# Kernel optimization log

Hardware: AMD Instinct MI355X
Metric: run time of the kernel (lower is better)

Reference implementation:

```python
import jax, jax.numpy as jnp
import numpy as np

N_NODES = 100000


def _gcn_conv(x, W, b, src, dst, n_nodes):
    # PyG GCNConv: linear transform, add self-loops, symmetric deg normalization,
    # scatter-add aggregation at target nodes, then bias.
    h = x @ W  # [N, out]
    loops = jnp.arange(n_nodes, dtype=src.dtype)
    src2 = jnp.concatenate([src, loops])
    dst2 = jnp.concatenate([dst, loops])
    ones = jnp.ones(src2.shape[0], dtype=h.dtype)
    deg = jax.ops.segment_sum(ones, dst2, num_segments=n_nodes)  # in-degree incl. self-loop
    dinv = jnp.where(deg > 0, jax.lax.rsqrt(deg), 0.0)
    norm = dinv[src2] * dinv[dst2]  # [E+N]
    msg = h[src2] * norm[:, None]  # gather + weight, [E+N, out]
    out = jax.ops.segment_sum(msg, dst2, num_segments=n_nodes)
    return out + b


def setup_inputs() -> dict:
    key = jax.random.key(0)
    k1, k2, k3, k4 = jax.random.split(key, 4)
    n, e, f, h, c = N_NODES, 3200000, 512, 16, 32
    x = jax.random.normal(k1, (n, f), dtype=jnp.float32)
    edge_index = jax.random.randint(k2, (2, e), 0, n, dtype=jnp.int64)
    W1 = jax.random.normal(k3, (f, h), dtype=jnp.float32) * (1.0 / np.sqrt(f))
    b1 = jnp.zeros((h,), dtype=jnp.float32)
    W2 = jax.random.normal(k4, (h, c), dtype=jnp.float32) * (1.0 / np.sqrt(h))
    b2 = jnp.zeros((c,), dtype=jnp.float32)
    return {"x": x, "edge_index": edge_index, "W1": W1, "b1": b1, "W2": W2, "b2": b2}


def reference(x, edge_index, W1, b1, W2, b2):
    src, dst = edge_index[0], edge_index[1]
    n = x.shape[0]
    h = _gcn_conv(x, W1, b1, src, dst, n)
    h = jax.nn.relu(h)
    h = _gcn_conv(h, W2, b2, src, dst, n)
    return jax.nn.log_softmax(h, axis=1)
```

## Files before the change

kernel.cpp:

```cpp
#include <hip/hip_runtime.h>
#include <hip/hip_bf16.h>


#define BK 128
#define BKSH 7
#define MAXNB 1024
#define CHUNK 12800

typedef __attribute__((ext_vector_type(8))) short bf16x8;
typedef __attribute__((ext_vector_type(4))) float f32x4;

__device__ __forceinline__ short f2b(float f) {
    unsigned u = __float_as_uint(f);
    return (short)((u + 0x7FFF + ((u >> 16) & 1)) >> 16);
}
__device__ __forceinline__ float b2f(unsigned short s) {
    return __uint_as_float(((unsigned)s) << 16);
}

__device__ __forceinline__ void load_lds16(const float* g, void* l) {
    __builtin_amdgcn_global_load_lds((const __attribute__((address_space(1))) void*)g,
                                     (__attribute__((address_space(3))) void*)l, 16, 0, 0);
}

__global__ __launch_bounds__(256) void k_zero_i(int* __restrict__ p, int n) {
    int i = blockIdx.x * 256 + threadIdx.x;
    if (i < n) p[i] = 0;
}

__global__ __launch_bounds__(256) void k_hist(const int* __restrict__ dst,
                                              int* __restrict__ gcnt, int E, int NB) {
    __shared__ int h[MAXNB];
    for (int t = threadIdx.x; t < NB; t += 256) h[t] = 0;
    __syncthreads();
    int e0 = blockIdx.x * CHUNK, e1 = min(E, e0 + CHUNK);
    for (int e = e0 + threadIdx.x; e < e1; e += 256)
        atomicAdd(&h[dst[e] >> BKSH], 1);
    __syncthreads();
    for (int t = threadIdx.x; t < NB; t += 256)
        if (h[t]) atomicAdd(&gcnt[t], h[t]);
}

__global__ __launch_bounds__(1024) void k_scan_nb(const int* __restrict__ gcnt,
                                                  int* __restrict__ goffs,
                                                  int* __restrict__ gcur, int NB, int E) {
    __shared__ int sm[1024];
    int tid = threadIdx.x;
    int c = (tid < NB) ? gcnt[tid] : 0;
    sm[tid] = c;
    __syncthreads();
    for (int o = 1; o < 1024; o <<= 1) {
        int t = (tid >= o) ? sm[tid - o] : 0;
        __syncthreads();
        sm[tid] += t;
        __syncthreads();
    }
    if (tid < NB) { int v = sm[tid] - c; goffs[tid] = v; gcur[tid] = v; }
    if (tid == 0) goffs[NB] = E;
}

__global__ __launch_bounds__(256) void k_fill2(const int* __restrict__ src,
                                               const int* __restrict__ dst,
                                               int* __restrict__ gcur,
                                               int* __restrict__ gq, int E, int NB) {
    __shared__ int h[MAXNB];
    __shared__ int base[MAXNB];
    for (int t = threadIdx.x; t < NB; t += 256) h[t] = 0;
    __syncthreads();
    int e0 = blockIdx.x * CHUNK, e1 = min(E, e0 + CHUNK);
    for (int e = e0 + threadIdx.x; e < e1; e += 256)
        atomicAdd(&h[dst[e] >> BKSH], 1);
    __syncthreads();
    for (int t = threadIdx.x; t < NB; t += 256) {
        int c = h[t];
        base[t] = c ? atomicAdd(&gcur[t], c) : 0;
    }
    __syncthreads();
    for (int t = threadIdx.x; t < NB; t += 256) h[t] = 0;
    __syncthreads();
    for (int e = e0 + threadIdx.x; e < e1; e += 256) {
        int d = dst[e], b = d >> BKSH;
        int loc = atomicAdd(&h[b], 1);
        gq[base[b] + loc] = (src[e] << BKSH) | (d & (BK - 1));
    }
}

__global__ __launch_bounds__(256) void k_sortb(const int* __restrict__ gq,
                                               const int* __restrict__ goffs,
                                               int* __restrict__ gq2,
                                               int* __restrict__ offs,
                                               float* __restrict__ dinv,
                                               int n, int E) {
    __shared__ int cnt[BK];
    __shared__ int cur[BK];
    int b = blockIdx.x;
    if (threadIdx.x < BK) cnt[threadIdx.x] = 0;
    __syncthreads();
    int p0 = goffs[b], p1 = goffs[b + 1];
    for (int p = p0 + threadIdx.x; p < p1; p += 256)
        atomicAdd(&cnt[gq[p] & (BK - 1)], 1);
    __syncthreads();
    if (threadIdx.x < BK) cur[threadIdx.x] = cnt[threadIdx.x];
    __syncthreads();
    for (int o = 1; o < BK; o <<= 1) {
        int v = (threadIdx.x < BK && threadIdx.x >= o) ? cur[threadIdx.x - o] : 0;
        __syncthreads();
        if (threadIdx.x < BK) cur[threadIdx.x] += v;
        __syncthreads();
    }
    if (threadIdx.x < BK) {
        int excl = cur[threadIdx.x] - cnt[threadIdx.x];
        int node = (b << BKSH) + threadIdx.x;
        if (node < n) {
            offs[node] = p0 + excl;
            dinv[node] = rsqrtf((float)(cnt[threadIdx.x] + 1));
        }
        cur[threadIdx.x] = excl;
    }
    if (b == 0 && threadIdx.x == 0) offs[n] = E;
    __syncthreads();
    for (int p = p0 + threadIdx.x; p < p1; p += 256) {
        int e = gq[p];
        int loc = atomicAdd(&cur[e & (BK - 1)], 1);
        gq2[p0 + loc] = e;
    }
}

__global__ __launch_bounds__(256) void k_gemm_mfma(const float* __restrict__ x,
                                                   const float* __restrict__ W1,
                                                   const float* __restrict__ dinv,
                                                   unsigned short* __restrict__ gs1,
                                                   int n) {
    const int lane = threadIdx.x & 63;
    const int r = lane & 15;
    const int g4 = lane >> 4;
    const int wid = blockIdx.x * 4 + (threadIdx.x >> 6);
    const int nw = gridDim.x * 4;

    bf16x8 wf[16];
#pragma unroll
    for (int s = 0; s < 16; ++s) {
        int kb = s * 32 + g4 * 8;
#pragma unroll
        for (int j = 0; j < 8; ++j)
            wf[s][j] = f2b(W1[(size_t)(kb + j) * 16 + r]);
    }

    const int ntiles = (n + 15) >> 4;
    for (int tile = wid; tile < ntiles; tile += nw) {
        int m0 = tile << 4;
        int arow = m0 + r;
        if (arow >= n) arow = n - 1;
        const float* xp = x + (size_t)arow * 512 + g4 * 8;
        f32x4 acc = {0.f, 0.f, 0.f, 0.f};
#pragma unroll
        for (int s = 0; s < 16; ++s) {
            float4 f0 = *reinterpret_cast<const float4*>(xp + s * 32);
            float4 f1 = *reinterpret_cast<const float4*>(xp + s * 32 + 4);
            bf16x8 ah;
            ah[0] = f2b(f0.x); ah[1] = f2b(f0.y); ah[2] = f2b(f0.z); ah[3] = f2b(f0.w);
            ah[4] = f2b(f1.x); ah[5] = f2b(f1.y); ah[6] = f2b(f1.z); ah[7] = f2b(f1.w);
            acc = __builtin_amdgcn_mfma_f32_16x16x32_bf16(ah, wf[s], acc, 0, 0, 0);
        }
#pragma unroll
        for (int j = 0; j < 4; ++j) {
            int crow = m0 + g4 * 4 + j;
            if (crow < n) {
                float dvv = dinv[crow];
                gs1[(size_t)crow * 16 + r] = (unsigned short)f2b(acc[j] * dvv);
            }
        }
    }
}

__global__ __launch_bounds__(256) void k_agg_b(const unsigned short* __restrict__ featb,
                                               const int* __restrict__ gq2,
                                               const int* __restrict__ offs,
                                               const float* __restrict__ dinv,
                                               const float* __restrict__ bias,
                                               unsigned short* __restrict__ out_b,
                                               float* __restrict__ out_f,
                                               int n, int relu_flag) {
    int t = blockIdx.x * 256 + threadIdx.x;
    int i = t >> 4, k = t & 15;
    if (i >= n) return;
    float acc = b2f(featb[(size_t)i * 16 + k]);
    int p = offs[i], p1 = offs[i + 1];
    for (; p + 4 <= p1; p += 4) {
        int s0 = gq2[p] >> BKSH, s1 = gq2[p + 1] >> BKSH;
        int s2 = gq2[p + 2] >> BKSH, s3 = gq2[p + 3] >> BKSH;
        float v0 = b2f(featb[(size_t)s0 * 16 + k]);
        float v1 = b2f(featb[(size_t)s1 * 16 + k]);
        float v2 = b2f(featb[(size_t)s2 * 16 + k]);
        float v3 = b2f(featb[(size_t)s3 * 16 + k]);
        acc += v0 + v1 + v2 + v3;
    }
    for (; p < p1; ++p)
        acc += b2f(featb[(size_t)(gq2[p] >> BKSH) * 16 + k]);
    float dvi = dinv[i];
    float v = dvi * acc;
    if (relu_flag) {
        v = fmaxf(v + bias[k], 0.f) * dvi;
        out_b[(size_t)i * 16 + k] = (unsigned short)f2b(v);
    } else {
        out_f[(size_t)i * 16 + k] = v;
    }
}

__global__ __launch_bounds__(256) void k_out(const float* __restrict__ a,
                                             const float* __restrict__ W2,
                                             const float* __restrict__ b2,
                                             float* __restrict__ out, int n) {
    __shared__ float Ws[16 * 33];
    __shared__ float bs[32];
    for (int t = threadIdx.x; t < 512; t += 256) Ws[(t >> 5) * 33 + (t & 31)] = W2[t];
    if (threadIdx.x < 32) bs[threadIdx.x] = b2[threadIdx.x];
    __syncthreads();
    int t = blockIdx.x * 256 + threadIdx.x;
    int i = t >> 5, c = t & 31;
    if (i >= n) return;
    const float4* ar = reinterpret_cast<const float4*>(a + (size_t)i * 16);
    float acc = bs[c];
#pragma unroll
    for (int kk = 0; kk < 4; ++kk) {
        float4 v = ar[kk];
        acc += v.x * Ws[(4 * kk + 0) * 33 + c];
        acc += v.y * Ws[(4 * kk + 1) * 33 + c];
        acc += v.z * Ws[(4 * kk + 2) * 33 + c];
        acc += v.w * Ws[(4 * kk + 3) * 33 + c];
    }
    float m = acc;
#pragma unroll
    for (int o = 16; o > 0; o >>= 1) m = fmaxf(m, __shfl_xor(m, o, 32));
    float p = expf(acc - m);
#pragma unroll
    for (int o = 16; o > 0; o >>= 1) p += __shfl_xor(p, o, 32);
    out[t] = acc - m - logf(p);
}

__global__ __launch_bounds__(256) void k_count(const int* __restrict__ dst,
                                               int* __restrict__ cnt, int E) {
    int e = blockIdx.x * 256 + threadIdx.x;
    if (e < E) atomicAdd(&cnt[dst[e]], 1);
}

__global__ __launch_bounds__(256) void k_dinv(const int* __restrict__ cnt,
                                              float* __restrict__ dinv, int n) {
    int i = blockIdx.x * 256 + threadIdx.x;
    if (i < n) dinv[i] = rsqrtf((float)(cnt[i] + 1));
}

__global__ __launch_bounds__(256) void k_gemm1(const float* __restrict__ x,
                                               const float* __restrict__ W1,
                                               const float* __restrict__ dinv,
                                               float* __restrict__ h1,
                                               float* __restrict__ r1self, int n) {
    __shared__ float Ws[8192];
    __shared__ float4 Xs[4][512];
    for (int t = threadIdx.x; t < 8192; t += 256) {
        int sa = t ^ (((t >> 9) & 1) << 4);
        Ws[sa] = W1[t];
    }
    __syncthreads();
    const int wave = threadIdx.x >> 6;
    const int lane = threadIdx.x & 63;
    const int q = lane & 15, g = lane >> 4;
    const int sr = lane >> 3, su = lane & 7;
    const int first = blockIdx.x * 4 + wave;
    const int stride = gridDim.x * 4;
    const int ngroups = (n + 7) >> 3;
    if (first >= ngroups) return;
    const int mygroups = (ngroups - first + stride - 1) / stride;
    const int T = mygroups * 4;
    char* xbase = (char*)(&Xs[wave][0]);
    auto stage = [&](int i) {
        int k = i >> 2, c = i & 3;
        int r0 = (first + k * stride) << 3;
        int row = r0 + sr;
        if (row >= n) row = n - 1;
        const float* gp = x + (size_t)row * 512 + c * 128 + su * 4;
        char* lb = xbase + (i & 1) * 4096;
#pragma unroll
        for (int m = 0; m < 4; ++m) load_lds16(gp + m * 32, lb + m * 1024);
    };
    stage(0);
    if (T > 1) stage(1);
    int issued = (T > 1) ? 2 : 1;
    float acc[8];
    const float4* xw = &Xs[wave][0];
    const int flip = (g & 1) << 4;
    for (int i = 0; i < T; ++i) {
        if (i < T - 1) asm volatile("s_waitcnt vmcnt(4)" ::: "memory");
        else           asm volatile("s_waitcnt vmcnt(0)" ::: "memory");
        int c = i & 3;
        const float4* xb = xw + (i & 1) * 256;
        if (c == 0) {
#pragma unroll
            for (int r = 0; r < 8; ++r) acc[r] = 0.f;
        }
        const int aW = 2048 * c + 512 * g + q;
#pragma unroll
        for (int t = 0; t < 8; ++t) {
            int tg = (t + g) & 7;
            float4 xv[8];
#pragma unroll
            for (int r = 0; r < 8; ++r) xv[r] = xb[g * 64 + r * 8 + tg];
            int a0 = aW + 64 * tg;
            float w0 = Ws[(a0) ^ flip];
            float w1 = Ws[(a0 + 16) ^ flip];
            float w2 = Ws[(a0 + 32) ^ flip];
            float w3 = Ws[(a0 + 48) ^ flip];
#pragma unroll
            for (int r = 0; r < 8; ++r)
                acc[r] += xv[r].x * w0 + xv[r].y * w1 + xv[r].z * w2 + xv[r].w * w3;
        }
        if (issued < T) { stage(issued); ++issued; }
        if (c == 3) {
            int r0 = (first + (i >> 2) * stride) << 3;
#pragma unroll
            for (int r = 0; r < 8; ++r) {
                acc[r] += __shfl_xor(acc[r], 16);
                acc[r] += __shfl_xor(acc[r], 32);
            }
            float v0 = 0.f, v1 = 0.f;
#pragma unroll
            for (int r = 0; r < 4; ++r)
                if (g == r) { v0 = acc[r]; v1 = acc[r + 4]; }
            int row0 = r0 + g, row1 = r0 + 4 + g;
            if (row0 < n) {
                h1[(size_t)row0 * 16 + q] = v0;
                if (r1self) { float dv = dinv[row0]; r1self[(size_t)row0 * 16 + q] = v0 * dv * dv; }
            }
            if (row1 < n) {
                h1[(size_t)row1 * 16 + q] = v1;
                if (r1self) { float dv = dinv[row1]; r1self[(size_t)row1 * 16 + q] = v1 * dv * dv; }
            }
        }
    }
}

__global__ __launch_bounds__(256) void k_scatter16(const int* __restrict__ src,
                                                   const int* __restrict__ dst,
                                                   const float* __restrict__ feat,
                                                   const float* __restrict__ dinv,
                                                   float* __restrict__ outf, int total) {
    int t = blockIdx.x * 256 + threadIdx.x;
    if (t >= total) return;
    int e = t >> 4, k = t & 15;
    int s = src[e], d = dst[e];
    float w = dinv[s] * dinv[d];
    unsafeAtomicAdd(&outf[(size_t)d * 16 + k], feat[(size_t)s * 16 + k] * w);
}

__global__ __launch_bounds__(256) void k_relu16(float* __restrict__ r1,
                                                const float* __restrict__ b1, int total) {
    int t = blockIdx.x * 256 + threadIdx.x;
    if (t < total) r1[t] = fmaxf(r1[t] + b1[t & 15], 0.f);
}

__global__ __launch_bounds__(256) void k_self16(const float* __restrict__ feat,
                                                const float* __restrict__ dinv,
                                                float* __restrict__ outf, int total) {
    int t = blockIdx.x * 256 + threadIdx.x;
    if (t >= total) return;
    float dv = dinv[t >> 4];
    outf[t] = feat[t] * dv * dv;
}

extern "C" void kernel_launch(void* const* d_in, const int* in_sizes, int n_in,
                              void* d_out, int out_size, void* d_ws, size_t ws_size,
                              hipStream_t stream) {
    const float* x  = (const float*)d_in[0];
    const int* ei   = (const int*)d_in[1];
    const float* W1 = (const float*)d_in[2];
    const float* b1 = (const float*)d_in[3];
    const float* W2 = (const float*)d_in[4];
    const float* b2 = (const float*)d_in[5];
    float* out = (float*)d_out;

    const int n = in_sizes[0] / 512;
    const int E = in_sizes[1] / 2;
    const int* src = ei;
    const int* dst = ei + E;
    const int NB = (n + BK - 1) >> BKSH;
    const int gfill = (E + CHUNK - 1) / CHUNK;

    float* ws = (float*)d_ws;

    size_t u_dinv  = 0;
    size_t u_foffs = u_dinv + n;
    size_t u_goffs = u_foffs + n + 1;
    size_t u_gcnt  = u_goffs + NB + 1;
    size_t u_gcur  = u_gcnt + NB;
    size_t u_gq    = u_gcur + NB;
    size_t u_gq2   = u_gq + (size_t)E;
    size_t u_h1    = u_gq2 + (size_t)E;
    size_t u_r1    = u_h1 + 16 * (size_t)n;
    size_t need    = (u_r1 + 16 * (size_t)n) * 4;

    if (ws_size >= need && NB <= MAXNB) {
        float* dinv = ws + u_dinv;
        int* offs   = (int*)(ws + u_foffs);
        int* goffs  = (int*)(ws + u_goffs);
        int* gcnt   = (int*)(ws + u_gcnt);
        int* gcur   = (int*)(ws + u_gcur);
        int* gq     = (int*)(ws + u_gq);
        int* gq2    = (int*)(ws + u_gq2);
        unsigned short* gs1b = (unsigned short*)(ws + u_h1);
        unsigned short* r1sb = (unsigned short*)(ws + u_r1);
        float* a_f  = ws + u_h1;

        k_zero_i <<<(NB + 255) / 256, 256, 0, stream>>>(gcnt, NB);
        k_hist   <<<gfill, 256, 0, stream>>>(dst, gcnt, E, NB);
        k_scan_nb<<<1, 1024, 0, stream>>>(gcnt, goffs, gcur, NB, E);
        k_fill2  <<<gfill, 256, 0, stream>>>(src, dst, gcur, gq, E, NB);
        k_sortb  <<<NB, 256, 0, stream>>>(gq, goffs, gq2, offs, dinv, n, E);
        k_gemm_mfma<<<1024, 256, 0, stream>>>(x, W1, dinv, gs1b, n);
        k_agg_b  <<<(n * 16 + 255) / 256, 256, 0, stream>>>(gs1b, gq2, offs, dinv, b1,
                                                            r1sb, nullptr, n, 1);
        k_agg_b  <<<(n * 16 + 255) / 256, 256, 0, stream>>>(r1sb, gq2, offs, dinv, b1,
                                                            nullptr, a_f, n, 0);
        k_out    <<<(n * 32 + 255) / 256, 256, 0, stream>>>(a_f, W2, b2, out, n);
    } else {
        float* dinv = ws;
        float* h1   = ws + n;
        float* r1   = ws + n + 16 * (size_t)n;
        int* cnt    = (int*)h1;
        float* agg2r = h1;

        const int total1 = E * 16;
        k_zero_i   <<<(n + 255) / 256, 256, 0, stream>>>(cnt, n);
        k_count    <<<(E + 255) / 256, 256, 0, stream>>>(dst, cnt, E);
        k_dinv     <<<(n + 255) / 256, 256, 0, stream>>>(cnt, dinv, n);
        k_gemm1    <<<1024, 256, 0, stream>>>(x, W1, dinv, h1, r1, n);
        k_scatter16<<<(total1 + 255) / 256, 256, 0, stream>>>(src, dst, h1, dinv, r1, total1);
        k_relu16   <<<(n * 16 + 255) / 256, 256, 0, stream>>>(r1, b1, n * 16);
        k_self16   <<<(n * 16 + 255) / 256, 256, 0, stream>>>(r1, dinv, agg2r, n * 16);
        k_scatter16<<<(total1 + 255) / 256, 256, 0, stream>>>(src, dst, r1, dinv, agg2r, total1);
        k_out      <<<(n * 32 + 255) / 256, 256, 0, stream>>>(agg2r, W2, b2, out, n);
    }
}
```

Measured before the change: 252.7 us.

## Fuse second aggregation with output GEMM and log-softmax; store pre-shifted sources

The second-layer aggregation kernel and the output linear+log_softmax kernel are merged into one kernel. Aggregated rows are staged in shared memory and each 16-thread group computes 32 logits and their log-softmax directly, which drops one launch and the fp32 intermediate round trip. The sorted edge list now stores the source index already shifted, so the per-edge shift in both aggregation passes goes away. Streaming reads of x, gq and gq2 use nontemporal loads to reduce cache pollution. The fused kernel adds a block barrier and per-thread matmul work.

New measurement: 255.2 us. Within noise of the previous version (+1.0%).

```diff
diff --git a/kernel.cpp b/kernel.cpp
--- a/kernel.cpp
+++ b/kernel.cpp
@@ -98,7 +98,7 @@
     __syncthreads();
     int p0 = goffs[b], p1 = goffs[b + 1];
     for (int p = p0 + threadIdx.x; p < p1; p += 256)
-        atomicAdd(&cnt[gq[p] & (BK - 1)], 1);
+        atomicAdd(&cnt[__builtin_nontemporal_load(gq + p) & (BK - 1)], 1);
     __syncthreads();
     if (threadIdx.x < BK) cur[threadIdx.x] = cnt[threadIdx.x];
     __syncthreads();
@@ -120,9 +120,9 @@
     if (b == 0 && threadIdx.x == 0) offs[n] = E;
     __syncthreads();
     for (int p = p0 + threadIdx.x; p < p1; p += 256) {
-        int e = gq[p];
+        int e = __builtin_nontemporal_load(gq + p);
         int loc = atomicAdd(&cur[e & (BK - 1)], 1);
-        gq2[p0 + loc] = e;
+        gq2[p0 + loc] = e >> BKSH;
     }
 }
 
@@ -155,11 +155,11 @@
         f32x4 acc = {0.f, 0.f, 0.f, 0.f};
 #pragma unroll
         for (int s = 0; s < 16; ++s) {
-            float4 f0 = *reinterpret_cast<const float4*>(xp + s * 32);
-            float4 f1 = *reinterpret_cast<const float4*>(xp + s * 32 + 4);
+            f32x4 f0 = __builtin_nontemporal_load(reinterpret_cast<const f32x4*>(xp + s * 32));
+            f32x4 f1 = __builtin_nontemporal_load(reinterpret_cast<const f32x4*>(xp + s * 32 + 4));
             bf16x8 ah;
-            ah[0] = f2b(f0.x); ah[1] = f2b(f0.y); ah[2] = f2b(f0.z); ah[3] = f2b(f0.w);
-            ah[4] = f2b(f1.x); ah[5] = f2b(f1.y); ah[6] = f2b(f1.z); ah[7] = f2b(f1.w);
+            ah[0] = f2b(f0[0]); ah[1] = f2b(f0[1]); ah[2] = f2b(f0[2]); ah[3] = f2b(f0[3]);
+            ah[4] = f2b(f1[0]); ah[5] = f2b(f1[1]); ah[6] = f2b(f1[2]); ah[7] = f2b(f1[3]);
             acc = __builtin_amdgcn_mfma_f32_16x16x32_bf16(ah, wf[s], acc, 0, 0, 0);
         }
 #pragma unroll
@@ -179,16 +179,17 @@
                                                const float* __restrict__ dinv,
                                                const float* __restrict__ bias,
                                                unsigned short* __restrict__ out_b,
-                                               float* __restrict__ out_f,
-                                               int n, int relu_flag) {
+                                               int n) {
     int t = blockIdx.x * 256 + threadIdx.x;
     int i = t >> 4, k = t & 15;
     if (i >= n) return;
     float acc = b2f(featb[(size_t)i * 16 + k]);
     int p = offs[i], p1 = offs[i + 1];
     for (; p + 4 <= p1; p += 4) {
-        int s0 = gq2[p] >> BKSH, s1 = gq2[p + 1] >> BKSH;
-        int s2 = gq2[p + 2] >> BKSH, s3 = gq2[p + 3] >> BKSH;
+        int s0 = __builtin_nontemporal_load(gq2 + p);
+        int s1 = __builtin_nontemporal_load(gq2 + p + 1);
+        int s2 = __builtin_nontemporal_load(gq2 + p + 2);
+        int s3 = __builtin_nontemporal_load(gq2 + p + 3);
         float v0 = b2f(featb[(size_t)s0 * 16 + k]);
         float v1 = b2f(featb[(size_t)s1 * 16 + k]);
         float v2 = b2f(featb[(size_t)s2 * 16 + k]);
@@ -196,46 +197,67 @@
         acc += v0 + v1 + v2 + v3;
     }
     for (; p < p1; ++p)
-        acc += b2f(featb[(size_t)(gq2[p] >> BKSH) * 16 + k]);
+        acc += b2f(featb[(size_t)__builtin_nontemporal_load(gq2 + p) * 16 + k]);
     float dvi = dinv[i];
-    float v = dvi * acc;
-    if (relu_flag) {
-        v = fmaxf(v + bias[k], 0.f) * dvi;
-        out_b[(size_t)i * 16 + k] = (unsigned short)f2b(v);
-    } else {
-        out_f[(size_t)i * 16 + k] = v;
-    }
-}
-
-__global__ __launch_bounds__(256) void k_out(const float* __restrict__ a,
-                                             const float* __restrict__ W2,
-                                             const float* __restrict__ b2,
-                                             float* __restrict__ out, int n) {
+    float v = fmaxf(dvi * acc + bias[k], 0.f) * dvi;
+    out_b[(size_t)i * 16 + k] = (unsigned short)f2b(v);
+}
+
+__global__ __launch_bounds__(256) void k_agg_out(const unsigned short* __restrict__ featb,
+                                                 const int* __restrict__ gq2,
+                                                 const int* __restrict__ offs,
+                                                 const float* __restrict__ dinv,
+                                                 const float* __restrict__ W2,
+                                                 const float* __restrict__ b2,
+                                                 float* __restrict__ out, int n) {
     __shared__ float Ws[16 * 33];
     __shared__ float bs[32];
+    __shared__ float As[16][17];
     for (int t = threadIdx.x; t < 512; t += 256) Ws[(t >> 5) * 33 + (t & 31)] = W2[t];
     if (threadIdx.x < 32) bs[threadIdx.x] = b2[threadIdx.x];
-    __syncthreads();
-    int t = blockIdx.x * 256 + threadIdx.x;
-    int i = t >> 5, c = t & 31;
-    if (i >= n) return;
-    const float4* ar = reinterpret_cast<const float4*>(a + (size_t)i * 16);
-    float acc = bs[c];
-#pragma unroll
-    for (int kk = 0; kk < 4; ++kk) {
-        float4 v = ar[kk];
-        acc += v.x * Ws[(4 * kk + 0) * 33 + c];
-        acc += v.y * Ws[(4 * kk + 1) * 33 + c];
-        acc += v.z * Ws[(4 * kk + 2) * 33 + c];
-        acc += v.w * Ws[(4 * kk + 3) * 33 + c];
-    }
-    float m = acc;
-#pragma unroll
-    for (int o = 16; o > 0; o >>= 1) m = fmaxf(m, __shfl_xor(m, o, 32));
-    float p = expf(acc - m);
-#pragma unroll
-    for (int o = 16; o > 0; o >>= 1) p += __shfl_xor(p, o, 32);
-    out[t] = acc - m - logf(p);
+
+    int t = blockIdx.x * 256 + threadIdx.x;
+    int i = t >> 4, k = t & 15, nl = threadIdx.x >> 4;
+    float acc = 0.f;
+    if (i < n) {
+        acc = b2f(featb[(size_t)i * 16 + k]);
+        int p = offs[i], p1 = offs[i + 1];
+        for (; p + 4 <= p1; p += 4) {
+            int s0 = __builtin_nontemporal_load(gq2 + p);
+            int s1 = __builtin_nontemporal_load(gq2 + p + 1);
+            int s2 = __builtin_nontemporal_load(gq2 + p + 2);
+            int s3 = __builtin_nontemporal_load(gq2 + p + 3);
+            float v0 = b2f(featb[(size_t)s0 * 16 + k]);
+            float v1 = b2f(featb[(size_t)s1 * 16 + k]);
+            float v2 = b2f(featb[(size_t)s2 * 16 + k]);
+            float v3 = b2f(featb[(size_t)s3 * 16 + k]);
+            acc += v0 + v1 + v2 + v3;
+        }
+        for (; p < p1; ++p)
+            acc += b2f(featb[(size_t)__builtin_nontemporal_load(gq2 + p) * 16 + k]);
+        acc *= dinv[i];
+    }
+    As[nl][k] = acc;
+    __syncthreads();
+    if (i < n) {
+        float v0 = bs[k], v1 = bs[k + 16];
+#pragma unroll
+        for (int kk = 0; kk < 16; ++kk) {
+            float a = As[nl][kk];
+            v0 += a * Ws[kk * 33 + k];
+            v1 += a * Ws[kk * 33 + k + 16];
+        }
+        float m = fmaxf(v0, v1);
+#pragma unroll
+        for (int o = 8; o > 0; o >>= 1) m = fmaxf(m, __shfl_xor(m, o, 16));
+        float pp = expf(v0 - m) + expf(v1 - m);
+#pragma unroll
+        for (int o = 8; o > 0; o >>= 1) pp += __shfl_xor(pp, o, 16);
+        float lg = logf(pp);
+        float* op = out + (size_t)i * 32;
+        op[k] = v0 - m - lg;
+        op[k + 16] = v1 - m - lg;
+    }
 }
 
 __global__ __launch_bounds__(256) void k_count(const int* __restrict__ dst,
@@ -367,6 +389,37 @@
     outf[t] = feat[t] * dv * dv;
 }
 
+__global__ __launch_bounds__(256) void k_out(const float* __restrict__ a,
+                                             const float* __restrict__ W2,
+                                             const float* __restrict__ b2,
+                                             float* __restrict__ out, int n) {
+    __shared__ float Ws[16 * 33];
+    __shared__ float bs[32];
+    for (int t = threadIdx.x; t < 512; t += 256) Ws[(t >> 5) * 33 + (t & 31)] = W2[t];
+    if (threadIdx.x < 32) bs[threadIdx.x] = b2[threadIdx.x];
+    __syncthreads();
+    int t = blockIdx.x * 256 + threadIdx.x;
+    int i = t >> 5, c = t & 31;
+    if (i >= n) return;
+    const float4* ar = reinterpret_cast<const float4*>(a + (size_t)i * 16);
+    float acc = bs[c];
+#pragma unroll
+    for (int kk = 0; kk < 4; ++kk) {
+        float4 v = ar[kk];
+        acc += v.x * Ws[(4 * kk + 0) * 33 + c];
+        acc += v.y * Ws[(4 * kk + 1) * 33 + c];
+        acc += v.z * Ws[(4 * kk + 2) * 33 + c];
+        acc += v.w * Ws[(4 * kk + 3) * 33 + c];
+    }
+    float m = acc;
+#pragma unroll
+    for (int o = 16; o > 0; o >>= 1) m = fmaxf(m, __shfl_xor(m, o, 32));
+    float p = expf(acc - m);
+#pragma unroll
+    for (int o = 16; o > 0; o >>= 1) p += __shfl_xor(p, o, 32);
+    out[t] = acc - m - logf(p);
+}
+
 extern "C" void kernel_launch(void* const* d_in, const int* in_sizes, int n_in,
                               void* d_out, int out_size, void* d_ws, size_t ws_size,
                               hipStream_t stream) {
@@ -408,7 +461,6 @@
         int* gq2    = (int*)(ws + u_gq2);
         unsigned short* gs1b = (unsigned short*)(ws + u_h1);
         unsigned short* r1sb = (unsigned short*)(ws + u_r1);
-        float* a_f  = ws + u_h1;
 
         k_zero_i <<<(NB + 255) / 256, 256, 0, stream>>>(gcnt, NB);
         k_hist   <<<gfill, 256, 0, stream>>>(dst, gcnt, E, NB);
@@ -417,10 +469,9 @@
         k_sortb  <<<NB, 256, 0, stream>>>(gq, goffs, gq2, offs, dinv, n, E);
         k_gemm_mfma<<<1024, 256, 0, stream>>>(x, W1, dinv, gs1b, n);
         k_agg_b  <<<(n * 16 + 255) / 256, 256, 0, stream>>>(gs1b, gq2, offs, dinv, b1,
-                                                            r1sb, nullptr, n, 1);
-        k_agg_b  <<<(n * 16 + 255) / 256, 256, 0, stream>>>(r1sb, gq2, offs, dinv, b1,
-                                                            nullptr, a_f, n, 0);
-        k_out    <<<(n * 32 + 255) / 256, 256, 0, stream>>>(a_f, W2, b2, out, n);
+                                                            r1sb, n);
+        k_agg_out<<<(n * 16 + 255) / 256, 256, 0, stream>>>(r1sb, gq2, offs, dinv,
+                                                            W2, b2, out, n);
     } else {
         float* dinv = ws;
         float* h1   = ws + n;
```
